# Optimization experiments

Hardware: AMD Instinct MI355X
Metric: run time of the kernel (lower is better)

The kernel has to match this reference:

```python
import jax, jax.numpy as jnp
import numpy as np


def conv1x1(x, W, b):
    # 1x1 Conv2d == per-pixel linear over channels. x: [B,C,H,W], W: [O,C], b: [O]
    return jnp.einsum('oc,bchw->bohw', W, x) + b[None, :, None, None]


def setup_inputs() -> dict:
    key = jax.random.key(0)
    ks = jax.random.split(key, 18)
    B, C, Hd, H, W = 16, 64, 64, 32, 32
    s = 0.05
    f = jax.random.normal
    return {
        'h': f(ks[0], (B, C, H, W), jnp.float32),
        'm': f(ks[1], (B, C, H, W), jnp.float32),
        'Wq': f(ks[2], (Hd, C), jnp.float32) * s,
        'bq': f(ks[3], (Hd,), jnp.float32) * s,
        'Wk': f(ks[4], (Hd, C), jnp.float32) * s,
        'bk': f(ks[5], (Hd,), jnp.float32) * s,
        'Wk2': f(ks[6], (Hd, C), jnp.float32) * s,
        'bk2': f(ks[7], (Hd,), jnp.float32) * s,
        'Wv': f(ks[8], (C, C), jnp.float32) * s,
        'bv': f(ks[9], (C,), jnp.float32) * s,
        'Wv2': f(ks[10], (C, C), jnp.float32) * s,
        'bv2': f(ks[11], (C,), jnp.float32) * s,
        'Wz': f(ks[12], (2 * C, 2 * C), jnp.float32) * s,
        'bz': f(ks[13], (2 * C,), jnp.float32) * s,
        'Wm': f(ks[14], (3 * C, 3 * C), jnp.float32) * s,
        'bm': f(ks[15], (3 * C,), jnp.float32) * s,
    }


def reference(h, m, Wq, bq, Wk, bk, Wk2, bk2, Wv, bv, Wv2, bv2, Wz, bz, Wm, bm):
    B, C, H, W = h.shape
    Hd = Wq.shape[0]
    N = H * W
    # Shared query from h
    Q_h = conv1x1(h, Wq, bq).reshape(B, Hd, N).transpose(0, 2, 1)  # [B,N,Hd]
    # Self-attention branch over h
    K_h = conv1x1(h, Wk, bk).reshape(B, Hd, N)                     # [B,Hd,N]
    A_h = jax.nn.softmax(jnp.einsum('bnd,bdm->bnm', Q_h, K_h), axis=-1)  # [B,N,N]
    V_h = conv1x1(h, Wv, bv).reshape(B, C, N)                      # [B,C,N]
    Z_h = jnp.einsum('bnm,bcm->bcn', A_h, V_h).reshape(B, C, H, W)
    # Cross-attention branch over memory m (same query Q_h)
    K_m = conv1x1(m, Wk2, bk2).reshape(B, Hd, N)
    A_m = jax.nn.softmax(jnp.einsum('bnd,bdm->bnm', Q_h, K_m), axis=-1)
    V_m = conv1x1(m, Wv2, bv2).reshape(B, C, N)
    Z_m = jnp.einsum('bnm,bcm->bcn', A_m, V_m).reshape(B, C, H, W)
    # Fuse and gated memory update
    Z = conv1x1(jnp.concatenate([Z_h, Z_m], axis=1), Wz, bz)       # [B,2C,H,W]
    combined = conv1x1(jnp.concatenate([Z, h], axis=1), Wm, bm)    # [B,3C,H,W]
    mo, mg, mi = combined[:, :C], combined[:, C:2 * C], combined[:, 2 * C:]
    mi = jax.nn.sigmoid(mi)
    new_m = (1 - mi) * m + mi * jnp.tanh(mg)
    new_h = jax.nn.sigmoid(mo) * new_m
    return (new_h, new_m)
```

## Files before the change

### kernel.cpp

```cpp
#include <hip/hip_runtime.h>

typedef unsigned short u16;
typedef unsigned int u32;
typedef __attribute__((ext_vector_type(8))) short bf16x8;
typedef __attribute__((ext_vector_type(4))) float f32x4;

#define MFMA(a, b, c) __builtin_amdgcn_mfma_f32_16x16x32_bf16((a), (b), (c), 0, 0, 0)

static __device__ __forceinline__ u16 f2bf(float x) {
  u32 u = __float_as_uint(x);
  u += 0x7FFFu + ((u >> 16) & 1u);
  return (u16)(u >> 16);
}
static __device__ __forceinline__ u32 packbf_t(float hi, float lo) {
  return __builtin_amdgcn_perm(__float_as_uint(hi), __float_as_uint(lo), 0x07060302u);
}
static __device__ __forceinline__ u32 packbf(float lo, float hi) {
  return (u32)f2bf(lo) | ((u32)f2bf(hi) << 16);
}

__global__ void prep_kernel(const float* __restrict__ Wq, const float* __restrict__ Wk,
                            const float* __restrict__ Wk2, const float* __restrict__ Wv,
                            const float* __restrict__ Wv2, const float* __restrict__ Wz,
                            const float* __restrict__ Wm, const float* __restrict__ bm,
                            u16* __restrict__ W5, u16* __restrict__ Wzb,
                            u16* __restrict__ Wmb, float* __restrict__ bmp) {
  const int id = blockIdx.x * 256 + threadIdx.x;
  if (id < 20480) {
    const int wi = id >> 12, e = id & 4095;
    const float* src = wi == 0 ? Wq : wi == 1 ? Wk : wi == 2 ? Wk2 : wi == 3 ? Wv : Wv2;
    W5[id] = f2bf(src[e]);
  } else if (id < 36864) {
    const int e = id - 20480;
    Wzb[e] = f2bf(Wz[e]);
  } else if (id < 73728) {
    const int e = id - 36864;
    const int p = e / 192, k = e % 192;
    const int hb2 = p / 96, r1 = p % 96, ctl = r1 / 48, r2 = r1 % 48;
    const int g = r2 >> 4, mm = r2 & 15;
    const int o = g * 64 + (hb2 * 2 + ctl) * 16 + mm;
    Wmb[p * 192 + k] = f2bf(Wm[o * 192 + k]);
  } else if (id < 73920) {
    const int p = id - 73728;
    const int hb2 = p / 96, r1 = p % 96, ctl = r1 / 48, r2 = r1 % 48;
    const int g = r2 >> 4, mm = r2 & 15;
    const int o = g * 64 + (hb2 * 2 + ctl) * 16 + mm;
    bmp[p] = bm[o];
  }
}

__global__ __launch_bounds__(256) void proj_kernel(
    const float* __restrict__ h, const float* __restrict__ m_,
    const float* __restrict__ bq, const float* __restrict__ bk,
    const float* __restrict__ bk2, const float* __restrict__ bv,
    const float* __restrict__ bv2, const u16* __restrict__ W5,
    u16* __restrict__ Qb, u16* __restrict__ Khb, u16* __restrict__ Kmb,
    u16* __restrict__ Vhb, u16* __restrict__ Vmb, u16* __restrict__ hbuf)
{
  const int b = blockIdx.y, n0 = blockIdx.x * 64, z = blockIdx.z;
  __shared__ __align__(16) u16 xt[64][72];
  const int tid = threadIdx.x;
  const float* __restrict__ X = z ? m_ : h;

  {
    const int px = tid & 63, c0 = (tid >> 6) * 16;
#pragma unroll
    for (int i = 0; i < 8; ++i) {
      const int c = c0 + 2 * i;
      const float f0 = X[(b * 64 + c) * 1024 + n0 + px];
      const float f1 = X[(b * 64 + c + 1) * 1024 + n0 + px];
      *(u32*)&xt[px][c] = packbf(f0, f1);
    }
  }
  __syncthreads();

  const int lane = tid & 63, w = tid >> 6;
  const int mm = lane & 15, q = lane >> 4;

  const bf16x8 xa0 = *(const bf16x8*)&xt[w * 16 + mm][q * 8];
  const bf16x8 xa1 = *(const bf16x8*)&xt[w * 16 + mm][32 + q * 8];

  auto qk_store = [&](u16* dst, const u16* Wb, const float* bias) {
#pragma unroll
    for (int ot = 0; ot < 4; ++ot) {
      const bf16x8 wb0 = *(const bf16x8*)(Wb + (ot * 16 + mm) * 64 + q * 8);
      const bf16x8 wb1 = *(const bf16x8*)(Wb + (ot * 16 + mm) * 64 + 32 + q * 8);
      const float4 b4 = *(const float4*)(bias + ot * 16 + q * 4);
      f32x4 d = {b4.x, b4.y, b4.z, b4.w};
      d = MFMA(wb0, xa0, d);
      d = MFMA(wb1, xa1, d);
      uint2 val;
      val.x = packbf(d[0], d[1]);
      val.y = packbf(d[2], d[3]);
      *(uint2*)(dst + (b * 1024 + n0 + w * 16 + mm) * 64 + ot * 16 + q * 4) = val;
    }
  };
  auto v_store = [&](u16* dst, const u16* Wb, const float* bias) {
#pragma unroll
    for (int ot = 0; ot < 4; ++ot) {
      const bf16x8 wb0 = *(const bf16x8*)(Wb + (ot * 16 + mm) * 64 + q * 8);
      const bf16x8 wb1 = *(const bf16x8*)(Wb + (ot * 16 + mm) * 64 + 32 + q * 8);
      const float bb = bias[ot * 16 + mm];
      f32x4 d = {bb, bb, bb, bb};
      d = MFMA(xa0, wb0, d);
      d = MFMA(xa1, wb1, d);
      uint2 val;
      val.x = packbf(d[0], d[1]);
      val.y = packbf(d[2], d[3]);
      *(uint2*)(dst + b * 65536 + blockIdx.x * 4096 + (ot * 16 + mm) * 64 +
                w * 16 + q * 4) = val;
    }
  };

  if (z == 0) {
    qk_store(Qb, W5, bq);
    qk_store(Khb, W5 + 4096, bk);
    v_store(Vhb, W5 + 3 * 4096, bv);
    const int px = tid >> 2, sg = tid & 3;
    u32* dst = (u32*)(hbuf + (b * 1024 + n0 + px) * 64 + sg * 16);
    const u16* srcr = &xt[px][sg * 16];
#pragma unroll
    for (int j = 0; j < 8; ++j) dst[j] = *(const u32*)(srcr + 2 * j);
  } else {
    qk_store(Kmb, W5 + 2 * 4096, bk2);
    v_store(Vmb, W5 + 4 * 4096, bv2);
  }
}

__global__ __launch_bounds__(256) void attn_kernel(
    const u16* __restrict__ Qb, const u16* __restrict__ Khb,
    const u16* __restrict__ Kmb, const u16* __restrict__ Vhb,
    const u16* __restrict__ Vmb, u16* __restrict__ Ztb)
{
  const int id = blockIdx.x;
  const int b = id & 15;
  const int br = (id >> 4) & 1;
  const int qh = id >> 5;
  const u16* __restrict__ K = (br ? Kmb : Khb) + b * 65536;
  const u16* __restrict__ V = (br ? Vmb : Vhb) + b * 65536;

  __shared__ __align__(16) u16 Kl[2][4096];
  __shared__ __align__(16) u16 Vl[2][4096];
  __shared__ __align__(16) u16 ps[4][16][40];

  const int tid = threadIdx.x, w = tid >> 6, lane = tid & 63;
  const int mm = lane & 15, q = lane >> 4, m7 = mm & 7;
  const int q0 = qh * 128 + w * 32;

  bf16x8 qa0[2], qa1[2];
#pragma unroll
  for (int qt = 0; qt < 2; ++qt) {
    const u16* Qp = Qb + (b * 1024 + q0 + qt * 16 + mm) * 64;
    qa0[qt] = *(const bf16x8*)(Qp + q * 8);
    qa1[qt] = *(const bf16x8*)(Qp + 32 + q * 8);
  }

  f32x4 z[2][4];
#pragma unroll
  for (int qt = 0; qt < 2; ++qt)
#pragma unroll
    for (int ct = 0; ct < 4; ++ct) z[qt][ct] = (f32x4){0.f, 0.f, 0.f, 0.f};
  float rp[2] = {0.f, 0.f};

  const int u0 = tid, u1 = 256 + tid;
  const int l0 = (((u0 & ~7) | ((u0 ^ (u0 >> 3)) & 7))) * 8;
  const int l1 = (((u1 & ~7) | ((u1 ^ (u1 >> 3)) & 7))) * 8;
  uint4 sk0, sk1, sv0, sv1;

  auto stage_load = [&](int kc) {
    const u16* Ks = K + kc * 4096;
    const u16* Vs = V + kc * 4096;
    sk0 = *(const uint4*)(Ks + u0 * 8);
    sk1 = *(const uint4*)(Ks + u1 * 8);
    sv0 = *(const uint4*)(Vs + u0 * 8);
    sv1 = *(const uint4*)(Vs + u1 * 8);
  };
  auto stage_store = [&](u16* Kd, u16* Vd) {
    *(uint4*)(Kd + l0) = sk0;
    *(uint4*)(Kd + l1) = sk1;
    *(uint4*)(Vd + l0) = sv0;
    *(uint4*)(Vd + l1) = sv1;
  };

  stage_load(0);
  stage_store(Kl[0], Vl[0]);
  __syncthreads();

  const u16* Kcur = Kl[0];
  const u16* Vcur = Vl[0];
  u16* Knxt = Kl[1];
  u16* Vnxt = Vl[1];

#pragma unroll 1
  for (int kc = 0; kc < 16; ++kc) {
    if (kc < 15) stage_load(kc + 1);

#pragma unroll
    for (int t2 = 0; t2 < 2; ++t2) {
      bf16x8 kf0[2], kf1[2], vf[4];
#pragma unroll
      for (int tt = 0; tt < 2; ++tt) {
        const u16* Kb = Kcur + (t2 * 32 + tt * 16 + mm) * 64;
        kf0[tt] = *(const bf16x8*)(Kb + ((q ^ m7) * 8));
        kf1[tt] = *(const bf16x8*)(Kb + (((q + 4) ^ m7) * 8));
      }
#pragma unroll
      for (int ct = 0; ct < 4; ++ct) {
        const u16* Vb = Vcur + (ct * 16 + mm) * 64;
        vf[ct] = *(const bf16x8*)(Vb + (((t2 * 4 + q) ^ m7) * 8));
      }

#pragma unroll
      for (int qt = 0; qt < 2; ++qt) {
#pragma unroll
        for (int tt = 0; tt < 2; ++tt) {
          f32x4 s = {0.f, 0.f, 0.f, 0.f};
          s = MFMA(kf0[tt], qa0[qt], s);
          s = MFMA(kf1[tt], qa1[qt], s);
          const float e0 = __expf(s[0]), e1 = __expf(s[1]);
          const float e2 = __expf(s[2]), e3 = __expf(s[3]);
          rp[qt] += (e0 + e1) + (e2 + e3);
          *(u32*)&ps[w][mm][tt * 16 + q * 4] = packbf_t(e1, e0);
          *(u32*)&ps[w][mm][tt * 16 + q * 4 + 2] = packbf_t(e3, e2);
        }
        const bf16x8 pb = *(const bf16x8*)&ps[w][mm][q * 8];
#pragma unroll
        for (int ct = 0; ct < 4; ++ct) z[qt][ct] = MFMA(vf[ct], pb, z[qt][ct]);
      }
    }

    if (kc < 15) stage_store(Knxt, Vnxt);
    __syncthreads();
    const u16* tk = Kcur; Kcur = Knxt; Knxt = (u16*)tk;
    const u16* tv = Vcur; Vcur = Vnxt; Vnxt = (u16*)tv;
  }

#pragma unroll
  for (int qt = 0; qt < 2; ++qt) {
    float v = rp[qt];
    v += __shfl_xor(v, 16);
    v += __shfl_xor(v, 32);
    const float rinv = __builtin_amdgcn_rcpf(v);
    u16* Zr = Ztb + (b * 1024 + q0 + qt * 16 + mm) * 128 + br * 64;
#pragma unroll
    for (int ct = 0; ct < 4; ++ct) {
      uint2 val;
      val.x = packbf(z[qt][ct][0] * rinv, z[qt][ct][1] * rinv);
      val.y = packbf(z[qt][ct][2] * rinv, z[qt][ct][3] * rinv);
      *(uint2*)(Zr + ct * 16 + q * 4) = val;
    }
  }
}

__global__ __launch_bounds__(256) void tail_kernel(
    const u16* __restrict__ Ztb, const u16* __restrict__ hbuf,
    const float* __restrict__ m_, const u16* __restrict__ Wzb,
    const float* __restrict__ bz, const u16* __restrict__ Wmb,
    const float* __restrict__ bmp, float* __restrict__ out)
{
  const int b = blockIdx.y, n0 = blockIdx.x * 32;
  __shared__ __align__(16) u16 zp[32][136];
  const int tid = threadIdx.x, lane = tid & 63, wv = tid >> 6;
  const int mm = lane & 15, q = lane >> 4;
  const int pxt = wv & 1, oh = wv >> 1;

  {
    bf16x8 za[4];
#pragma unroll
    for (int ks = 0; ks < 4; ++ks)
      za[ks] = *(const bf16x8*)(Ztb + (b * 1024 + n0 + pxt * 16 + mm) * 128 +
                                ks * 32 + q * 8);
#pragma unroll
    for (int ot = 0; ot < 4; ++ot) {
      const int o0 = oh * 64 + ot * 16;
      const float4 b4 = *(const float4*)(bz + o0 + q * 4);
      f32x4 d = {b4.x, b4.y, b4.z, b4.w};
#pragma unroll
      for (int ks = 0; ks < 4; ++ks) {
        const bf16x8 wb = *(const bf16x8*)(Wzb + (o0 + mm) * 128 + ks * 32 + q * 8);
        d = MFMA(wb, za[ks], d);
      }
      uint2 val;
      val.x = packbf(d[0], d[1]);
      val.y = packbf(d[2], d[3]);
      *(uint2*)&zp[pxt * 16 + mm][o0 + q * 4] = val;
    }
  }
  __syncthreads();

  {
    const int hb2 = oh;
    bf16x8 fa[6];
#pragma unroll
    for (int ks = 0; ks < 4; ++ks)
      fa[ks] = *(const bf16x8*)&zp[pxt * 16 + mm][ks * 32 + q * 8];
    {
      const u16* hp = hbuf + (b * 1024 + n0 + pxt * 16 + mm) * 64;
      fa[4] = *(const bf16x8*)(hp + q * 8);
      fa[5] = *(const bf16x8*)(hp + 32 + q * 8);
    }
    f32x4 dd[6];
#pragma unroll
    for (int j = 0; j < 6; ++j) {
      const int p = hb2 * 96 + j * 16 + mm;
      const float bb = bmp[p];
      f32x4 d = {bb, bb, bb, bb};
#pragma unroll
      for (int ks = 0; ks < 6; ++ks) {
        const bf16x8 wb = *(const bf16x8*)(Wmb + p * 192 + ks * 32 + q * 8);
        d = MFMA(fa[ks], wb, d);
      }
      dd[j] = d;
    }
#pragma unroll
    for (int ctl = 0; ctl < 2; ++ctl) {
      const int c = (hb2 * 2 + ctl) * 16 + mm;
      const int px = n0 + pxt * 16 + q * 4;
      const float4 mold = *(const float4*)(m_ + (b * 64 + c) * 1024 + px);
      float4 nh, nm;
#pragma unroll
      for (int r = 0; r < 4; ++r) {
        const float xo = dd[ctl * 3 + 0][r];
        const float xg = dd[ctl * 3 + 1][r];
        const float xi = dd[ctl * 3 + 2][r];
        const float si = __builtin_amdgcn_rcpf(1.f + __expf(-xi));
        const float th = 1.f - 2.f * __builtin_amdgcn_rcpf(__expf(2.f * xg) + 1.f);
        const float so = __builtin_amdgcn_rcpf(1.f + __expf(-xo));
        const float mo = ((const float*)&mold)[r];
        const float nmv = (1.f - si) * mo + si * th;
        ((float*)&nm)[r] = nmv;
        ((float*)&nh)[r] = so * nmv;
      }
      *(float4*)(out + (b * 64 + c) * 1024 + px) = nh;
      *(float4*)(out + 1048576 + (b * 64 + c) * 1024 + px) = nm;
    }
  }
}

extern "C" void kernel_launch(void* const* d_in, const int* in_sizes, int n_in,
                              void* d_out, int out_size, void* d_ws, size_t ws_size,
                              hipStream_t stream) {
  const float* h   = (const float*)d_in[0];
  const float* m   = (const float*)d_in[1];
  const float* Wq  = (const float*)d_in[2];
  const float* bq  = (const float*)d_in[3];
  const float* Wk  = (const float*)d_in[4];
  const float* bk  = (const float*)d_in[5];
  const float* Wk2 = (const float*)d_in[6];
  const float* bk2 = (const float*)d_in[7];
  const float* Wv  = (const float*)d_in[8];
  const float* bv  = (const float*)d_in[9];
  const float* Wv2 = (const float*)d_in[10];
  const float* bv2 = (const float*)d_in[11];
  const float* Wz  = (const float*)d_in[12];
  const float* bz  = (const float*)d_in[13];
  const float* Wm  = (const float*)d_in[14];
  const float* bm  = (const float*)d_in[15];
  float* out = (float*)d_out;

  char* ws = (char*)d_ws;
  const size_t MB = 1024 * 1024;
  u16* Qb   = (u16*)(ws + 0 * MB);
  u16* Khb  = (u16*)(ws + 2 * MB);
  u16* Kmb  = (u16*)(ws + 4 * MB);
  u16* Vhb  = (u16*)(ws + 6 * MB);
  u16* Vmb  = (u16*)(ws + 8 * MB);
  u16* hbuf = (u16*)(ws + 10 * MB);
  u16* Ztb  = (u16*)(ws + 12 * MB);
  u16* W5   = (u16*)(ws + 16 * MB);
  u16* Wzb  = (u16*)(ws + 16 * MB + 40960);
  u16* Wmb  = (u16*)(ws + 16 * MB + 73728);
  float* bmp = (float*)(ws + 16 * MB + 147456);

  prep_kernel<<<289, 256, 0, stream>>>(Wq, Wk, Wk2, Wv, Wv2, Wz, Wm, bm,
                                       W5, Wzb, Wmb, bmp);
  proj_kernel<<<dim3(16, 16, 2), 256, 0, stream>>>(h, m, bq, bk, bk2, bv, bv2, W5,
                                                   Qb, Khb, Kmb, Vhb, Vmb, hbuf);
  attn_kernel<<<256, 256, 0, stream>>>(Qb, Khb, Kmb, Vhb, Vmb, Ztb);
  tail_kernel<<<dim3(32, 16), 256, 0, stream>>>(Ztb, hbuf, m, Wzb, bz, Wmb, bmp, out);
}
```

Measured before the change: 141.7 us.

## Split attention keys across waves with cross-wave reduction and doubled grid

The attention kernel now gives each wave a slice of keys within each chunk for all 64 queries of the block, where before each wave owned 32 queries over every key. The score exponentials feed straight into a 16x16x16 MFMA as register operands, which removes the per-wave shared-memory round trip for P. Partial outputs and row sums are then reduced across the four waves through shared memory. Blocks cover 64 queries instead of 128, so the grid doubles to 512 blocks for more parallelism. The costs are bf16 rounding of the partial sums before the reduction, an extra barrier and reduction pass, and padded LDS rows in place of the XOR swizzle.

```diff
diff --git a/kernel.cpp b/kernel.cpp
--- a/kernel.cpp
+++ b/kernel.cpp
@@ -3,9 +3,11 @@
 typedef unsigned short u16;
 typedef unsigned int u32;
 typedef __attribute__((ext_vector_type(8))) short bf16x8;
+typedef __attribute__((ext_vector_type(4))) short bf16x4;
 typedef __attribute__((ext_vector_type(4))) float f32x4;
 
 #define MFMA(a, b, c) __builtin_amdgcn_mfma_f32_16x16x32_bf16((a), (b), (c), 0, 0, 0)
+#define MFMA16(a, b, c) __builtin_amdgcn_mfma_f32_16x16x16bf16_1k((a), (b), (c), 0, 0, 0)
 
 static __device__ __forceinline__ u16 f2bf(float x) {
   u32 u = __float_as_uint(x);
@@ -139,116 +141,121 @@
   const u16* __restrict__ K = (br ? Kmb : Khb) + b * 65536;
   const u16* __restrict__ V = (br ? Vmb : Vhb) + b * 65536;
 
-  __shared__ __align__(16) u16 Kl[2][4096];
-  __shared__ __align__(16) u16 Vl[2][4096];
-  __shared__ __align__(16) u16 ps[4][16][40];
+  __shared__ __align__(16) u16 pool[18432];
+  __shared__ float rsw[4][64];
+  u16* const Kl = pool;
+  u16* const Vl = pool + 9216;
 
   const int tid = threadIdx.x, w = tid >> 6, lane = tid & 63;
-  const int mm = lane & 15, q = lane >> 4, m7 = mm & 7;
-  const int q0 = qh * 128 + w * 32;
-
-  bf16x8 qa0[2], qa1[2];
-#pragma unroll
-  for (int qt = 0; qt < 2; ++qt) {
+  const int mm = lane & 15, q = lane >> 4;
+  const int q0 = qh * 64;
+
+  bf16x8 qb0[4], qb1[4];
+#pragma unroll
+  for (int qt = 0; qt < 4; ++qt) {
     const u16* Qp = Qb + (b * 1024 + q0 + qt * 16 + mm) * 64;
-    qa0[qt] = *(const bf16x8*)(Qp + q * 8);
-    qa1[qt] = *(const bf16x8*)(Qp + 32 + q * 8);
-  }
-
-  f32x4 z[2][4];
-#pragma unroll
-  for (int qt = 0; qt < 2; ++qt)
+    qb0[qt] = *(const bf16x8*)(Qp + q * 8);
+    qb1[qt] = *(const bf16x8*)(Qp + 32 + q * 8);
+  }
+
+  f32x4 z[4][4];
+#pragma unroll
+  for (int qt = 0; qt < 4; ++qt)
 #pragma unroll
     for (int ct = 0; ct < 4; ++ct) z[qt][ct] = (f32x4){0.f, 0.f, 0.f, 0.f};
-  float rp[2] = {0.f, 0.f};
-
-  const int u0 = tid, u1 = 256 + tid;
-  const int l0 = (((u0 & ~7) | ((u0 ^ (u0 >> 3)) & 7))) * 8;
-  const int l1 = (((u1 & ~7) | ((u1 ^ (u1 >> 3)) & 7))) * 8;
+  float rp[4] = {0.f, 0.f, 0.f, 0.f};
+
+  const int so0 = (tid >> 3) * 72 + (tid & 7) * 8;
+  const int so1 = so0 + 32 * 72;
   uint4 sk0, sk1, sv0, sv1;
-
   auto stage_load = [&](int kc) {
     const u16* Ks = K + kc * 4096;
     const u16* Vs = V + kc * 4096;
-    sk0 = *(const uint4*)(Ks + u0 * 8);
-    sk1 = *(const uint4*)(Ks + u1 * 8);
-    sv0 = *(const uint4*)(Vs + u0 * 8);
-    sv1 = *(const uint4*)(Vs + u1 * 8);
+    sk0 = *(const uint4*)(Ks + tid * 8);
+    sk1 = *(const uint4*)(Ks + tid * 8 + 2048);
+    sv0 = *(const uint4*)(Vs + tid * 8);
+    sv1 = *(const uint4*)(Vs + tid * 8 + 2048);
   };
-  auto stage_store = [&](u16* Kd, u16* Vd) {
-    *(uint4*)(Kd + l0) = sk0;
-    *(uint4*)(Kd + l1) = sk1;
-    *(uint4*)(Vd + l0) = sv0;
-    *(uint4*)(Vd + l1) = sv1;
+  auto stage_store = [&](int buf) {
+    u16* Kd = Kl + buf * 4608;
+    u16* Vd = Vl + buf * 4608;
+    *(uint4*)(Kd + so0) = sk0;
+    *(uint4*)(Kd + so1) = sk1;
+    *(uint4*)(Vd + so0) = sv0;
+    *(uint4*)(Vd + so1) = sv1;
   };
 
   stage_load(0);
-  stage_store(Kl[0], Vl[0]);
+  stage_store(0);
   __syncthreads();
 
-  const u16* Kcur = Kl[0];
-  const u16* Vcur = Vl[0];
-  u16* Knxt = Kl[1];
-  u16* Vnxt = Vl[1];
-
+  int cur = 0;
 #pragma unroll 1
   for (int kc = 0; kc < 16; ++kc) {
     if (kc < 15) stage_load(kc + 1);
 
-#pragma unroll
-    for (int t2 = 0; t2 < 2; ++t2) {
-      bf16x8 kf0[2], kf1[2], vf[4];
-#pragma unroll
-      for (int tt = 0; tt < 2; ++tt) {
-        const u16* Kb = Kcur + (t2 * 32 + tt * 16 + mm) * 64;
-        kf0[tt] = *(const bf16x8*)(Kb + ((q ^ m7) * 8));
-        kf1[tt] = *(const bf16x8*)(Kb + (((q + 4) ^ m7) * 8));
-      }
-#pragma unroll
-      for (int ct = 0; ct < 4; ++ct) {
-        const u16* Vb = Vcur + (ct * 16 + mm) * 64;
-        vf[ct] = *(const bf16x8*)(Vb + (((t2 * 4 + q) ^ m7) * 8));
-      }
-
-#pragma unroll
-      for (int qt = 0; qt < 2; ++qt) {
-#pragma unroll
-        for (int tt = 0; tt < 2; ++tt) {
-          f32x4 s = {0.f, 0.f, 0.f, 0.f};
-          s = MFMA(kf0[tt], qa0[qt], s);
-          s = MFMA(kf1[tt], qa1[qt], s);
-          const float e0 = __expf(s[0]), e1 = __expf(s[1]);
-          const float e2 = __expf(s[2]), e3 = __expf(s[3]);
-          rp[qt] += (e0 + e1) + (e2 + e3);
-          *(u32*)&ps[w][mm][tt * 16 + q * 4] = packbf_t(e1, e0);
-          *(u32*)&ps[w][mm][tt * 16 + q * 4 + 2] = packbf_t(e3, e2);
-        }
-        const bf16x8 pb = *(const bf16x8*)&ps[w][mm][q * 8];
-#pragma unroll
-        for (int ct = 0; ct < 4; ++ct) z[qt][ct] = MFMA(vf[ct], pb, z[qt][ct]);
-      }
-    }
-
-    if (kc < 15) stage_store(Knxt, Vnxt);
+    const u16* Kc = Kl + cur * 4608;
+    const u16* Vc = Vl + cur * 4608;
+    const bf16x8 kf0 = *(const bf16x8*)(Kc + (w * 16 + mm) * 72 + q * 8);
+    const bf16x8 kf1 = *(const bf16x8*)(Kc + (w * 16 + mm) * 72 + 32 + q * 8);
+    bf16x4 vf[4];
+#pragma unroll
+    for (int ct = 0; ct < 4; ++ct)
+      vf[ct] = *(const bf16x4*)(Vc + (ct * 16 + mm) * 72 + w * 16 + q * 4);
+
+#pragma unroll
+    for (int qt = 0; qt < 4; ++qt) {
+      f32x4 s = {0.f, 0.f, 0.f, 0.f};
+      s = MFMA(kf0, qb0[qt], s);
+      s = MFMA(kf1, qb1[qt], s);
+      const float e0 = __expf(s[0]), e1 = __expf(s[1]);
+      const float e2 = __expf(s[2]), e3 = __expf(s[3]);
+      rp[qt] += (e0 + e1) + (e2 + e3);
+      union { u32 u[2]; bf16x4 v; } pb;
+      pb.u[0] = packbf_t(e1, e0);
+      pb.u[1] = packbf_t(e3, e2);
+#pragma unroll
+      for (int ct = 0; ct < 4; ++ct) z[qt][ct] = MFMA16(vf[ct], pb.v, z[qt][ct]);
+    }
+
+    if (kc < 15) stage_store(cur ^ 1);
     __syncthreads();
-    const u16* tk = Kcur; Kcur = Knxt; Knxt = (u16*)tk;
-    const u16* tv = Vcur; Vcur = Vnxt; Vnxt = (u16*)tv;
-  }
-
-#pragma unroll
-  for (int qt = 0; qt < 2; ++qt) {
+    cur ^= 1;
+  }
+
+  u16* const zcb = pool;
+#pragma unroll
+  for (int qt = 0; qt < 4; ++qt) {
     float v = rp[qt];
     v += __shfl_xor(v, 16);
     v += __shfl_xor(v, 32);
-    const float rinv = __builtin_amdgcn_rcpf(v);
-    u16* Zr = Ztb + (b * 1024 + q0 + qt * 16 + mm) * 128 + br * 64;
+    if (q == 0) rsw[w][qt * 16 + mm] = v;
 #pragma unroll
     for (int ct = 0; ct < 4; ++ct) {
       uint2 val;
-      val.x = packbf(z[qt][ct][0] * rinv, z[qt][ct][1] * rinv);
-      val.y = packbf(z[qt][ct][2] * rinv, z[qt][ct][3] * rinv);
-      *(uint2*)(Zr + ct * 16 + q * 4) = val;
-    }
+      val.x = packbf_t(z[qt][ct][1], z[qt][ct][0]);
+      val.y = packbf_t(z[qt][ct][3], z[qt][ct][2]);
+      *(uint2*)(zcb + w * 4352 + (qt * 16 + mm) * 68 + ct * 16 + q * 4) = val;
+    }
+  }
+  __syncthreads();
+
+  const int c2 = tid & 31, qr = tid >> 5;
+#pragma unroll
+  for (int i = 0; i < 8; ++i) {
+    const int query = qr + i * 8;
+    const float rt = rsw[0][query] + rsw[1][query] + rsw[2][query] + rsw[3][query];
+    const float rinv = __builtin_amdgcn_rcpf(rt);
+    float vlo = 0.f, vhi = 0.f;
+#pragma unroll
+    for (int ww = 0; ww < 4; ++ww) {
+      const u32 u = *(const u32*)(zcb + ww * 4352 + query * 68 + c2 * 2);
+      vlo += __uint_as_float(u << 16);
+      vhi += __uint_as_float(u & 0xffff0000u);
+    }
+    vlo *= rinv;
+    vhi *= rinv;
+    *(u32*)(Ztb + (b * 1024 + q0 + query) * 128 + br * 64 + c2 * 2) = packbf_t(vhi, vlo);
   }
 }
 
@@ -376,6 +383,6 @@
                                        W5, Wzb, Wmb, bmp);
   proj_kernel<<<dim3(16, 16, 2), 256, 0, stream>>>(h, m, bq, bk, bk2, bv, bv2, W5,
                                                    Qb, Khb, Kmb, Vhb, Vmb, hbuf);
-  attn_kernel<<<256, 256, 0, stream>>>(Qb, Khb, Kmb, Vhb, Vmb, Ztb);
+  attn_kernel<<<512, 256, 0, stream>>>(Qb, Khb, Kmb, Vhb, Vmb, Ztb);
   tail_kernel<<<dim3(32, 16), 256, 0, stream>>>(Ztb, hbuf, m, Wzb, bz, Wmb, bmp, out);
 }
```

Result: faster. 136.0 us (-4.0%).
